# Optimization experiments

Measured on AMD Instinct MI355X. Metric: run time of the kernel, lower is better.

## Reference

```python
import jax, jax.numpy as jnp
import numpy as np

HIDDEN = 1024
N_HEADS = 16
HEAD_DIM = HIDDEN // N_HEADS
WINDOW = 256  # symmetric window: keys j with i - W//2 <= j <= i + W//2
BATCH, SEQ = 2, 2048


def setup_inputs() -> dict:
    key = jax.random.key(0)
    ks = jax.random.split(key, 9)
    s = 0.02
    return {
        "x":  jax.random.normal(ks[0], (BATCH, SEQ, HIDDEN), dtype=jnp.float32),
        "wq": jax.random.normal(ks[1], (HIDDEN, HIDDEN), dtype=jnp.float32) * s,
        "bq": jnp.zeros((HIDDEN,), dtype=jnp.float32),
        "wk": jax.random.normal(ks[2], (HIDDEN, HIDDEN), dtype=jnp.float32) * s,
        "bk": jnp.zeros((HIDDEN,), dtype=jnp.float32),
        "wv": jax.random.normal(ks[3], (HIDDEN, HIDDEN), dtype=jnp.float32) * s,
        "bv": jnp.zeros((HIDDEN,), dtype=jnp.float32),
        "wo": jax.random.normal(ks[4], (HIDDEN, HIDDEN), dtype=jnp.float32) * s,
        "bo": jnp.zeros((HIDDEN,), dtype=jnp.float32),
    }


def reference(x, wq, bq, wk, bk, wv, bv, wo, bo):
    B, S, Hs = x.shape
    scale = HEAD_DIM ** -0.5

    def proj(w, b):
        # [B,S,Hs] -> [B,H,S,D]
        return (x @ w + b).reshape(B, S, N_HEADS, HEAD_DIM).transpose(0, 2, 1, 3)

    q = proj(wq, bq)
    k = proj(wk, bk)
    v = proj(wv, bv)

    # Clipped sliding window == band-masked full attention (identical softmax weights).
    scores = jnp.einsum('bhid,bhjd->bhij', q, k) * scale  # [B,H,S,S]
    i = jnp.arange(S)[:, None]
    j = jnp.arange(S)[None, :]
    band = (j >= i - WINDOW // 2) & (j <= i + WINDOW // 2)
    scores = jnp.where(band, scores, -jnp.inf)
    attn = jax.nn.softmax(scores, axis=-1)
    out = jnp.einsum('bhij,bhjd->bhid', attn, v)  # [B,H,S,D]
    out = out.transpose(0, 2, 1, 3).reshape(B, S, Hs)
    return out @ wo + bo
```

## Files before the change

### kernel.cpp

```cpp
#include <hip/hip_runtime.h>
#include <hip/hip_bf16.h>
#include <stdint.h>

#define BATCH 2
#define SEQ   2048
#define HID   1024
#define NH    16
#define HD    64
#define W2    128

using bhalf8 = __attribute__((ext_vector_type(8))) short;
using fvec4  = __attribute__((ext_vector_type(4))) float;
using u16x8  = __attribute__((ext_vector_type(8))) unsigned short;

__device__ __forceinline__ unsigned short f2bf(float f) {
    union { float f; unsigned int u; } c; c.f = f;
    unsigned int u = c.u;
    u += 0x7FFFu + ((u >> 16) & 1u);
    return (unsigned short)(u >> 16);
}

__device__ __forceinline__ fvec4 zero4() {
    fvec4 z = {0.f, 0.f, 0.f, 0.f};
    return z;
}

__device__ __forceinline__ void load_lds16(const void* g, void* l) {
    __builtin_amdgcn_global_load_lds(
        (const __attribute__((address_space(1))) void*)g,
        (__attribute__((address_space(3))) void*)l, 16, 0, 0);
}


__global__ __launch_bounds__(256) void k_convert_x(const float* __restrict__ x,
                                                   unsigned short* __restrict__ xb) {
    int i = (blockIdx.x * 256 + threadIdx.x) * 8;
    float4 a = *(const float4*)(x + i);
    float4 b = *(const float4*)(x + i + 4);
    u16x8 o;
    o[0] = f2bf(a.x); o[1] = f2bf(a.y); o[2] = f2bf(a.z); o[3] = f2bf(a.w);
    o[4] = f2bf(b.x); o[5] = f2bf(b.y); o[6] = f2bf(b.z); o[7] = f2bf(b.w);
    *(u16x8*)(xb + i) = o;
}

__global__ __launch_bounds__(256) void k_transpose_w(
    const float* __restrict__ w0, const float* __restrict__ w1,
    const float* __restrict__ w2, const float* __restrict__ w3,
    unsigned short* __restrict__ t0, unsigned short* __restrict__ t1,
    unsigned short* __restrict__ t2, unsigned short* __restrict__ t3) {
    int z = blockIdx.z;
    const float* src = (z == 0) ? w0 : (z == 1) ? w1 : (z == 2) ? w2 : w3;
    unsigned short* dst = (z == 0) ? t0 : (z == 1) ? t1 : (z == 2) ? t2 : t3;
    __shared__ float tile[32][33];
    int n0 = blockIdx.x * 32, k0 = blockIdx.y * 32;
    int tx = threadIdx.x, ty = threadIdx.y;
#pragma unroll
    for (int r = 0; r < 4; ++r)
        tile[ty + 8 * r][tx] = src[(size_t)(k0 + ty + 8 * r) * HID + n0 + tx];
    __syncthreads();
#pragma unroll
    for (int r = 0; r < 4; ++r)
        dst[(size_t)(n0 + ty + 8 * r) * HID + k0 + tx] = f2bf(tile[tx][ty + 8 * r]);
}


__device__ __forceinline__ void stage_tile64(const unsigned short* __restrict__ A,
                                             const unsigned short* __restrict__ Bt,
                                             int m0, int n0, int k0,
                                             unsigned short* As, unsigned short* Bs,
                                             int t) {
#pragma unroll
    for (int i = 0; i < 2; ++i) {
        int chunk = t + 512 * i;
        int row = chunk >> 3, ch = chunk & 7;
        int chs = ch ^ (row & 7);
        load_lds16(A + (size_t)(m0 + row) * HID + k0 + chs * 8, As + chunk * 8);
        load_lds16(Bt + (size_t)(n0 + row) * HID + k0 + chs * 8, Bs + chunk * 8);
    }
}

__device__ __forceinline__ void gemm_tile8(const unsigned short* __restrict__ A,
                                           const unsigned short* __restrict__ Bt,
                                           int m0, int n0,
                                           unsigned short* As, unsigned short* Bs,
                                           fvec4 acc[4][2]) {
    const int t = threadIdx.x;
    const int lane = t & 63;
    const int wid = t >> 6;
    const int wr = wid >> 2, wc = wid & 3;
    const int c16 = lane & 15, g = lane >> 4;

#pragma unroll
    for (int mi = 0; mi < 4; ++mi)
#pragma unroll
        for (int ni = 0; ni < 2; ++ni) acc[mi][ni] = zero4();

    stage_tile64(A, Bt, m0, n0, 0, As, Bs, t);

    int cur = 0;
    for (int k0 = 0; k0 < HID; k0 += 64) {
        asm volatile("s_waitcnt vmcnt(0)" ::: "memory");
        __builtin_amdgcn_sched_barrier(0);
        __builtin_amdgcn_s_barrier();

        if (k0 + 64 < HID)
            stage_tile64(A, Bt, m0, n0, k0 + 64,
                         As + (cur ^ 1) * 8192, Bs + (cur ^ 1) * 8192, t);

        const unsigned short* Ab = As + cur * 8192;
        const unsigned short* Bb = Bs + cur * 8192;
        bhalf8 af[2][4], bf[2][2];
#pragma unroll
        for (int ks = 0; ks < 2; ++ks) {
#pragma unroll
            for (int i = 0; i < 4; ++i) {
                int ra = wr * 64 + i * 16 + c16;
                af[ks][i] = *(const bhalf8*)(Ab + ra * 64 + ((4 * ks + g) ^ (ra & 7)) * 8);
            }
#pragma unroll
            for (int i = 0; i < 2; ++i) {
                int rb = wc * 32 + i * 16 + c16;
                bf[ks][i] = *(const bhalf8*)(Bb + rb * 64 + ((4 * ks + g) ^ (rb & 7)) * 8);
            }
        }
        __builtin_amdgcn_s_setprio(1);
#pragma unroll
        for (int ks = 0; ks < 2; ++ks)
#pragma unroll
            for (int mi = 0; mi < 4; ++mi)
#pragma unroll
                for (int ni = 0; ni < 2; ++ni)
                    acc[mi][ni] = __builtin_amdgcn_mfma_f32_16x16x32_bf16(
                        af[ks][mi], bf[ks][ni], acc[mi][ni], 0, 0, 0);
        __builtin_amdgcn_s_setprio(0);
        cur ^= 1;
    }
}

__global__ __launch_bounds__(512, 4) void k_gemm_qkv(
    const unsigned short* __restrict__ xb,
    const unsigned short* __restrict__ wqt, const unsigned short* __restrict__ wkt,
    const unsigned short* __restrict__ wvt,
    const float* __restrict__ bq, const float* __restrict__ bk, const float* __restrict__ bv,
    unsigned short* __restrict__ qb, unsigned short* __restrict__ kbuf,
    unsigned short* __restrict__ vt) {
    __shared__ unsigned short SH[2][2 * 128 * 64];
    const int z = blockIdx.z;
    const unsigned short* Bt = (z == 0) ? wqt : (z == 1) ? wkt : wvt;
    const float* bias = (z == 0) ? bq : (z == 1) ? bk : bv;
    const int m0 = blockIdx.y * 128, n0 = blockIdx.x * 128;
    fvec4 acc[4][2];
    gemm_tile8(xb, Bt, m0, n0, SH[0], SH[1], acc);

    const int t = threadIdx.x, lane = t & 63, wid = t >> 6;
    const int wr = wid >> 2, wc = wid & 3, c16 = lane & 15, g = lane >> 4;

    if (z != 2) {
#pragma unroll
        for (int mi = 0; mi < 4; ++mi) {
#pragma unroll
            for (int ni = 0; ni < 2; ++ni) {
                int gcol = n0 + wc * 32 + ni * 16 + c16;
                int h = gcol >> 6, d = gcol & 63;
                float bsv = bias[gcol];
#pragma unroll
                for (int r = 0; r < 4; ++r) {
                    int grow = m0 + wr * 64 + mi * 16 + 4 * g + r;
                    int b = grow >> 11, s = grow & (SEQ - 1);
                    float v = acc[mi][ni][r] + bsv;
                    if (z == 0)
                        qb[((size_t)(b * NH + h) * SEQ + s) * HD + d] = f2bf(v * 0.125f);
                    else
                        kbuf[((size_t)(b * NH + h) * SEQ + s) * HD + d] = f2bf(v);
                }
            }
        }
    } else {
        unsigned short* VL = &SH[0][0];
        __syncthreads();
#pragma unroll
        for (int mi = 0; mi < 4; ++mi)
#pragma unroll
            for (int ni = 0; ni < 2; ++ni) {
                int dl = wc * 32 + ni * 16 + c16;
                float bsv = bias[n0 + dl];
#pragma unroll
                for (int r = 0; r < 4; ++r) {
                    int sl = wr * 64 + mi * 16 + 4 * g + r;
                    VL[dl * 132 + sl] = f2bf(acc[mi][ni][r] + bsv);
                }
            }
        __syncthreads();
        const int b = m0 >> 11, sbase = m0 & (SEQ - 1);
#pragma unroll
        for (int it = 0; it < 4; ++it) {
            int slot = t + 512 * it;
            int dl = slot >> 4, ch = slot & 15;
            int gcol = n0 + dl;
            int h = gcol >> 6, d = gcol & 63;
            u16x8 v = *(const u16x8*)(VL + dl * 132 + ch * 8);
            *(u16x8*)(vt + ((size_t)(b * NH + h) * HD + d) * SEQ + sbase + ch * 8) = v;
        }
    }
}

__global__ __launch_bounds__(512, 4) void k_gemm_out(
    const unsigned short* __restrict__ attn, const unsigned short* __restrict__ wot,
    const float* __restrict__ bo, float* __restrict__ out) {
    __shared__ unsigned short SH[2][2 * 128 * 64];
    const int m0 = blockIdx.y * 128, n0 = blockIdx.x * 128;
    fvec4 acc[4][2];
    gemm_tile8(attn, wot, m0, n0, SH[0], SH[1], acc);

    const int lane = threadIdx.x & 63, wid = threadIdx.x >> 6;
    const int wr = wid >> 2, wc = wid & 3, c16 = lane & 15, g = lane >> 4;
#pragma unroll
    for (int mi = 0; mi < 4; ++mi) {
#pragma unroll
        for (int ni = 0; ni < 2; ++ni) {
            int gcol = n0 + wc * 32 + ni * 16 + c16;
            float bsv = bo[gcol];
#pragma unroll
            for (int r = 0; r < 4; ++r) {
                int grow = m0 + wr * 64 + mi * 16 + 4 * g + r;
                out[(size_t)grow * HID + gcol] = acc[mi][ni][r] + bsv;
            }
        }
    }
}

__global__ __launch_bounds__(256) void k_attn(
    const unsigned short* __restrict__ qb, const unsigned short* __restrict__ kbuf,
    const unsigned short* __restrict__ vt, unsigned short* __restrict__ attn) {
    const int bh = blockIdx.y;
    const int wid = threadIdx.x >> 6, lane = threadIdx.x & 63;
    const int g = lane >> 4, c16 = lane & 15;
    const int q0 = blockIdx.x * 64 + wid * 16;

    const unsigned short* Qp = qb + (size_t)bh * SEQ * HD;
    const unsigned short* Kp = kbuf + (size_t)bh * SEQ * HD;
    const unsigned short* Vp = vt + (size_t)bh * HD * SEQ;

    bhalf8 qf0, qf1;
    {
        const unsigned short* p = Qp + (size_t)(q0 + c16) * HD + g * 8;
        qf0 = *(const bhalf8*)p;
        qf1 = *(const bhalf8*)(p + 32);
    }
    fvec4 acc[4];
#pragma unroll
    for (int i = 0; i < 4; ++i) acc[i] = zero4();
    float mq = -1e30f;
    float sq = 0.f;

    const int ia = q0 + c16;
    int kstart = q0 - W2; if (kstart < 0) kstart = 0; kstart &= ~31;
    int kend = q0 + 15 + W2; if (kend > SEQ - 1) kend = SEQ - 1;

    const int sl1 = ((2 * g) & 3) * 16 + c16;
    const int sl2 = ((2 * g + 1) & 3) * 16 + c16;

    for (int t0 = kstart; t0 <= kend; t0 += 32) {
        fvec4 st0 = zero4(), st1 = zero4();
        {
            const unsigned short* kp = Kp + (size_t)(t0 + c16) * HD + g * 8;
            bhalf8 ka = *(const bhalf8*)kp;
            bhalf8 ka2 = *(const bhalf8*)(kp + 32);
            st0 = __builtin_amdgcn_mfma_f32_16x16x32_bf16(ka, qf0, st0, 0, 0, 0);
            st0 = __builtin_amdgcn_mfma_f32_16x16x32_bf16(ka2, qf1, st0, 0, 0, 0);
        }
        {
            const unsigned short* kp = Kp + (size_t)(t0 + 16 + c16) * HD + g * 8;
            bhalf8 kb = *(const bhalf8*)kp;
            bhalf8 kb2 = *(const bhalf8*)(kp + 32);
            st1 = __builtin_amdgcn_mfma_f32_16x16x32_bf16(kb, qf0, st1, 0, 0, 0);
            st1 = __builtin_amdgcn_mfma_f32_16x16x32_bf16(kb2, qf1, st1, 0, 0, 0);
        }
#pragma unroll
        for (int r = 0; r < 4; ++r) {
            int j0 = t0 + 4 * g + r, j1 = j0 + 16;
            if (j0 < ia - W2 || j0 > ia + W2) st0[r] = -1e30f;
            if (j1 < ia - W2 || j1 > ia + W2) st1[r] = -1e30f;
        }
        float pm = fmaxf(fmaxf(fmaxf(st0[0], st0[1]), fmaxf(st0[2], st0[3])),
                         fmaxf(fmaxf(st1[0], st1[1]), fmaxf(st1[2], st1[3])));
        pm = fmaxf(pm, __shfl_xor(pm, 16));
        pm = fmaxf(pm, __shfl_xor(pm, 32));
        float mn = fmaxf(mq, pm);
        float f = __expf(mq - mn);
        mq = mn;
        float p0[4], p1[4];
        float psum = 0.f;
#pragma unroll
        for (int r = 0; r < 4; ++r) {
            p0[r] = __expf(st0[r] - mn);
            p1[r] = __expf(st1[r] - mn);
            psum += p0[r] + p1[r];
        }
        sq = sq * f + psum;
#pragma unroll
        for (int db = 0; db < 4; ++db) acc[db] *= f;

        unsigned int a01 = (unsigned int)f2bf(p0[0]) | ((unsigned int)f2bf(p0[1]) << 16);
        unsigned int a23 = (unsigned int)f2bf(p0[2]) | ((unsigned int)f2bf(p0[3]) << 16);
        unsigned int b01 = (unsigned int)f2bf(p1[0]) | ((unsigned int)f2bf(p1[1]) << 16);
        unsigned int b23 = (unsigned int)f2bf(p1[2]) | ((unsigned int)f2bf(p1[3]) << 16);
        unsigned int A01 = (unsigned int)__shfl((int)a01, sl1);
        unsigned int A23 = (unsigned int)__shfl((int)a23, sl1);
        unsigned int A01b = (unsigned int)__shfl((int)a01, sl2);
        unsigned int A23b = (unsigned int)__shfl((int)a23, sl2);
        unsigned int B01 = (unsigned int)__shfl((int)b01, sl1);
        unsigned int B23 = (unsigned int)__shfl((int)b23, sl1);
        unsigned int B01b = (unsigned int)__shfl((int)b01, sl2);
        unsigned int B23b = (unsigned int)__shfl((int)b23, sl2);
        union { unsigned int u[4]; bhalf8 v; } pb;
        pb.u[0] = (g < 2) ? A01 : B01;
        pb.u[1] = (g < 2) ? A23 : B23;
        pb.u[2] = (g < 2) ? A01b : B01b;
        pb.u[3] = (g < 2) ? A23b : B23b;

#pragma unroll
        for (int db = 0; db < 4; ++db) {
            const unsigned short* vp = Vp + (size_t)(db * 16 + c16) * SEQ + t0 + g * 8;
            bhalf8 vf = *(const bhalf8*)vp;
            acc[db] = __builtin_amdgcn_mfma_f32_16x16x32_bf16(vf, pb.v, acc[db], 0, 0, 0);
        }
    }

    sq += __shfl_xor(sq, 16);
    sq += __shfl_xor(sq, 32);
    float inv = 1.f / sq;

    const int b = bh >> 4, h = bh & 15;
    const int si = q0 + c16;
#pragma unroll
    for (int db = 0; db < 4; ++db)
#pragma unroll
        for (int r = 0; r < 4; ++r) {
            int d = db * 16 + 4 * g + r;
            attn[((size_t)(b * SEQ) + si) * HID + h * HD + d] = f2bf(acc[db][r] * inv);
        }
}


extern "C" void kernel_launch(void* const* d_in, const int* in_sizes, int n_in,
                              void* d_out, int out_size, void* d_ws, size_t ws_size,
                              hipStream_t stream) {
    const float* x  = (const float*)d_in[0];
    const float* wq = (const float*)d_in[1];
    const float* bq = (const float*)d_in[2];
    const float* wk = (const float*)d_in[3];
    const float* bk = (const float*)d_in[4];
    const float* wv = (const float*)d_in[5];
    const float* bv = (const float*)d_in[6];
    const float* wo = (const float*)d_in[7];
    const float* bo = (const float*)d_in[8];
    float* out = (float*)d_out;

    char* ws = (char*)d_ws;
    unsigned short* xb   = (unsigned short*)(ws);
    unsigned short* wqt  = (unsigned short*)(ws + (8u << 20));
    unsigned short* wkt  = wqt + 1024 * 1024;
    unsigned short* wvt  = wkt + 1024 * 1024;
    unsigned short* wot  = wvt + 1024 * 1024;
    unsigned short* qb   = wot + 1024 * 1024;
    unsigned short* kbuf = qb + 4u * 1024 * 1024;
    unsigned short* vt   = kbuf + 4u * 1024 * 1024;
    unsigned short* attn = vt + 4u * 1024 * 1024;

    k_convert_x<<<dim3(2048), dim3(256), 0, stream>>>(x, xb);
    k_transpose_w<<<dim3(32, 32, 4), dim3(32, 8), 0, stream>>>(wq, wk, wv, wo,
                                                               wqt, wkt, wvt, wot);
    k_gemm_qkv<<<dim3(8, 32, 3), dim3(512), 0, stream>>>(xb, wqt, wkt, wvt,
                                                         bq, bk, bv, qb, kbuf, vt);
    k_attn<<<dim3(SEQ / 64, BATCH * NH), dim3(256), 0, stream>>>(qb, kbuf, vt, attn);
    k_gemm_out<<<dim3(8, 32), dim3(512), 0, stream>>>(attn, wot, bo, out);
}
```

Measured before the change: 177.4 us.

## Merge prep kernels, prefetch K/V in attention loop, vectorize output stores

Fuses the x conversion and weight transpose into a single launch to save one kernel launch. The attention loop now loads the next K and V tiles into registers before computing the current tile, so global-load latency overlaps with the MFMA and softmax work. The attention output is written as 4-element vector stores instead of scalar bf16 stores. Double-buffering raises register pressure in the attention kernel, which could lower occupancy.

```diff
diff --git a/kernel.cpp b/kernel.cpp
--- a/kernel.cpp
+++ b/kernel.cpp
@@ -12,6 +12,7 @@
 using bhalf8 = __attribute__((ext_vector_type(8))) short;
 using fvec4  = __attribute__((ext_vector_type(4))) float;
 using u16x8  = __attribute__((ext_vector_type(8))) unsigned short;
+using u16x4  = __attribute__((ext_vector_type(4))) unsigned short;
 
 __device__ __forceinline__ unsigned short f2bf(float f) {
     union { float f; unsigned int u; } c; c.f = f;
@@ -31,36 +32,37 @@
         (__attribute__((address_space(3))) void*)l, 16, 0, 0);
 }
 
-
-__global__ __launch_bounds__(256) void k_convert_x(const float* __restrict__ x,
-                                                   unsigned short* __restrict__ xb) {
-    int i = (blockIdx.x * 256 + threadIdx.x) * 8;
-    float4 a = *(const float4*)(x + i);
-    float4 b = *(const float4*)(x + i + 4);
-    u16x8 o;
-    o[0] = f2bf(a.x); o[1] = f2bf(a.y); o[2] = f2bf(a.z); o[3] = f2bf(a.w);
-    o[4] = f2bf(b.x); o[5] = f2bf(b.y); o[6] = f2bf(b.z); o[7] = f2bf(b.w);
-    *(u16x8*)(xb + i) = o;
-}
-
-__global__ __launch_bounds__(256) void k_transpose_w(
+__global__ __launch_bounds__(256) void k_prep(
+    const float* __restrict__ x, unsigned short* __restrict__ xb,
     const float* __restrict__ w0, const float* __restrict__ w1,
     const float* __restrict__ w2, const float* __restrict__ w3,
     unsigned short* __restrict__ t0, unsigned short* __restrict__ t1,
     unsigned short* __restrict__ t2, unsigned short* __restrict__ t3) {
-    int z = blockIdx.z;
-    const float* src = (z == 0) ? w0 : (z == 1) ? w1 : (z == 2) ? w2 : w3;
-    unsigned short* dst = (z == 0) ? t0 : (z == 1) ? t1 : (z == 2) ? t2 : t3;
-    __shared__ float tile[32][33];
-    int n0 = blockIdx.x * 32, k0 = blockIdx.y * 32;
-    int tx = threadIdx.x, ty = threadIdx.y;
-#pragma unroll
-    for (int r = 0; r < 4; ++r)
-        tile[ty + 8 * r][tx] = src[(size_t)(k0 + ty + 8 * r) * HID + n0 + tx];
-    __syncthreads();
-#pragma unroll
-    for (int r = 0; r < 4; ++r)
-        dst[(size_t)(n0 + ty + 8 * r) * HID + k0 + tx] = f2bf(tile[tx][ty + 8 * r]);
+    const int bx = blockIdx.x, tid = threadIdx.x;
+    if (bx < 2048) {
+        int i = (bx * 256 + tid) * 8;
+        float4 a = *(const float4*)(x + i);
+        float4 b = *(const float4*)(x + i + 4);
+        u16x8 o;
+        o[0] = f2bf(a.x); o[1] = f2bf(a.y); o[2] = f2bf(a.z); o[3] = f2bf(a.w);
+        o[4] = f2bf(b.x); o[5] = f2bf(b.y); o[6] = f2bf(b.z); o[7] = f2bf(b.w);
+        *(u16x8*)(xb + i) = o;
+    } else {
+        int idx = bx - 2048;
+        int z = idx >> 10, rem = idx & 1023;
+        int n0 = (rem & 31) * 32, k0 = (rem >> 5) * 32;
+        const float* src = (z == 0) ? w0 : (z == 1) ? w1 : (z == 2) ? w2 : w3;
+        unsigned short* dst = (z == 0) ? t0 : (z == 1) ? t1 : (z == 2) ? t2 : t3;
+        __shared__ float tile[32][33];
+        int tx = tid & 31, ty = tid >> 5;
+#pragma unroll
+        for (int r = 0; r < 4; ++r)
+            tile[ty + 8 * r][tx] = src[(size_t)(k0 + ty + 8 * r) * HID + n0 + tx];
+        __syncthreads();
+#pragma unroll
+        for (int r = 0; r < 4; ++r)
+            dst[(size_t)(n0 + ty + 8 * r) * HID + k0 + tx] = f2bf(tile[tx][ty + 8 * r]);
+    }
 }
 
 
@@ -229,6 +231,22 @@
     }
 }
 
+__device__ __forceinline__ void attn_loadK(const unsigned short* __restrict__ Kp,
+                                           int t0, int c16, int g, bhalf8 k[4]) {
+    const unsigned short* kp0 = Kp + (size_t)(t0 + c16) * HD + g * 8;
+    k[0] = *(const bhalf8*)kp0;
+    k[1] = *(const bhalf8*)(kp0 + 32);
+    const unsigned short* kp1 = kp0 + 16 * HD;
+    k[2] = *(const bhalf8*)kp1;
+    k[3] = *(const bhalf8*)(kp1 + 32);
+}
+__device__ __forceinline__ void attn_loadV(const unsigned short* __restrict__ Vp,
+                                           int t0, int c16, int g, bhalf8 v[4]) {
+#pragma unroll
+    for (int db = 0; db < 4; ++db)
+        v[db] = *(const bhalf8*)(Vp + (size_t)(db * 16 + c16) * SEQ + t0 + g * 8);
+}
+
 __global__ __launch_bounds__(256) void k_attn(
     const unsigned short* __restrict__ qb, const unsigned short* __restrict__ kbuf,
     const unsigned short* __restrict__ vt, unsigned short* __restrict__ attn) {
@@ -260,22 +278,21 @@
     const int sl1 = ((2 * g) & 3) * 16 + c16;
     const int sl2 = ((2 * g + 1) & 3) * 16 + c16;
 
+    bhalf8 kc[4], vc[4], kn[4], vn[4];
+    attn_loadK(Kp, kstart, c16, g, kc);
+    attn_loadV(Vp, kstart, c16, g, vc);
+
     for (int t0 = kstart; t0 <= kend; t0 += 32) {
+        int tn = (t0 + 32 <= kend) ? t0 + 32 : t0;
+        attn_loadK(Kp, tn, c16, g, kn);
+        attn_loadV(Vp, tn, c16, g, vn);
+
         fvec4 st0 = zero4(), st1 = zero4();
-        {
-            const unsigned short* kp = Kp + (size_t)(t0 + c16) * HD + g * 8;
-            bhalf8 ka = *(const bhalf8*)kp;
-            bhalf8 ka2 = *(const bhalf8*)(kp + 32);
-            st0 = __builtin_amdgcn_mfma_f32_16x16x32_bf16(ka, qf0, st0, 0, 0, 0);
-            st0 = __builtin_amdgcn_mfma_f32_16x16x32_bf16(ka2, qf1, st0, 0, 0, 0);
-        }
-        {
-            const unsigned short* kp = Kp + (size_t)(t0 + 16 + c16) * HD + g * 8;
-            bhalf8 kb = *(const bhalf8*)kp;
-            bhalf8 kb2 = *(const bhalf8*)(kp + 32);
-            st1 = __builtin_amdgcn_mfma_f32_16x16x32_bf16(kb, qf0, st1, 0, 0, 0);
-            st1 = __builtin_amdgcn_mfma_f32_16x16x32_bf16(kb2, qf1, st1, 0, 0, 0);
-        }
+        st0 = __builtin_amdgcn_mfma_f32_16x16x32_bf16(kc[0], qf0, st0, 0, 0, 0);
+        st0 = __builtin_amdgcn_mfma_f32_16x16x32_bf16(kc[1], qf1, st0, 0, 0, 0);
+        st1 = __builtin_amdgcn_mfma_f32_16x16x32_bf16(kc[2], qf0, st1, 0, 0, 0);
+        st1 = __builtin_amdgcn_mfma_f32_16x16x32_bf16(kc[3], qf1, st1, 0, 0, 0);
+
 #pragma unroll
         for (int r = 0; r < 4; ++r) {
             int j0 = t0 + 4 * g + r, j1 = j0 + 16;
@@ -320,11 +337,11 @@
         pb.u[3] = (g < 2) ? A23b : B23b;
 
 #pragma unroll
-        for (int db = 0; db < 4; ++db) {
-            const unsigned short* vp = Vp + (size_t)(db * 16 + c16) * SEQ + t0 + g * 8;
-            bhalf8 vf = *(const bhalf8*)vp;
-            acc[db] = __builtin_amdgcn_mfma_f32_16x16x32_bf16(vf, pb.v, acc[db], 0, 0, 0);
-        }
+        for (int db = 0; db < 4; ++db)
+            acc[db] = __builtin_amdgcn_mfma_f32_16x16x32_bf16(vc[db], pb.v, acc[db], 0, 0, 0);
+
+#pragma unroll
+        for (int i = 0; i < 4; ++i) { kc[i] = kn[i]; vc[i] = vn[i]; }
     }
 
     sq += __shfl_xor(sq, 16);
@@ -333,13 +350,14 @@
 
     const int b = bh >> 4, h = bh & 15;
     const int si = q0 + c16;
-#pragma unroll
-    for (int db = 0; db < 4; ++db)
-#pragma unroll
-        for (int r = 0; r < 4; ++r) {
-            int d = db * 16 + 4 * g + r;
-            attn[((size_t)(b * SEQ) + si) * HID + h * HD + d] = f2bf(acc[db][r] * inv);
-        }
+    unsigned short* orow = attn + ((size_t)(b * SEQ) + si) * HID + h * HD;
+#pragma unroll
+    for (int db = 0; db < 4; ++db) {
+        u16x4 o;
+#pragma unroll
+        for (int r = 0; r < 4; ++r) o[r] = f2bf(acc[db][r] * inv);
+        *(u16x4*)(orow + db * 16 + 4 * g) = o;
+    }
 }
 
 
@@ -368,9 +386,8 @@
     unsigned short* vt   = kbuf + 4u * 1024 * 1024;
     unsigned short* attn = vt + 4u * 1024 * 1024;
 
-    k_convert_x<<<dim3(2048), dim3(256), 0, stream>>>(x, xb);
-    k_transpose_w<<<dim3(32, 32, 4), dim3(32, 8), 0, stream>>>(wq, wk, wv, wo,
-                                                               wqt, wkt, wvt, wot);
+    k_prep<<<dim3(6144), dim3(256), 0, stream>>>(x, xb, wq, wk, wv, wo,
+                                                 wqt, wkt, wvt, wot);
     k_gemm_qkv<<<dim3(8, 32, 3), dim3(512), 0, stream>>>(xb, wqt, wkt, wvt,
                                                          bq, bk, bv, qb, kbuf, vt);
     k_attn<<<dim3(SEQ / 64, BATCH * NH), dim3(256), 0, stream>>>(qb, kbuf, vt, attn);
```

Measured after the change: 181.9 us. 1.03x slower.
